# Optimization experiments

Measured on AMD Instinct MI355X. Metric: run time of the kernel, lower is better.

The kernel has to match this reference:

```python
import jax, jax.numpy as jnp
import numpy as np

B, M, L, D = 4, 128, 512, 768
NEG = -1e30


def setup_inputs() -> dict:
    key = jax.random.key(0)
    k1, k2 = jax.random.split(key)
    h = jax.random.normal(k1, (B, L, D), dtype=jnp.float32)
    mention_masks = jax.random.randint(k2, (B, M, L), 0, 2, dtype=jnp.int32)
    return {"h": h, "mention_masks": mention_masks}


def reference(h, mention_masks):
    # h: [B, L, D]; mention_masks: [B, M, L] (0/1)
    # Faithful to: m = (mask == 0).float() * -1e30; (m + h).max(dim=2)
    m = (mention_masks == 0).astype(h.dtype) * NEG          # [B, M, L]
    # broadcast add then max over token dim L -> [B, M, D]
    mention_reprs = jnp.max(h[:, None, :, :] + m[:, :, :, None], axis=2)
    return mention_reprs
```

## Files before the change

kernel.cpp:

```cpp
#include <hip/hip_runtime.h>

#define BB 4
#define MM 128
#define LL 512
#define DD 768
#define NEGF (-1e30f)

__global__ __launch_bounds__(256, 3) void mention_max_part(
    const float* __restrict__ h, const int* __restrict__ mask,
    float* __restrict__ ws)
{
    const int lane = threadIdx.x & 63;
    const int wave = threadIdx.x >> 6;
    const int dch  = blockIdx.x;
    const int mch  = blockIdx.y >> 2;
    const int lh   = blockIdx.y & 3;
    const int b    = blockIdx.z;

    const int d0 = dch * 256 + lane * 4;
    const int m0 = mch * 8;
    const int l0 = lh * 128 + wave * 32;

    const int lclamp = (l0 + lane < LL) ? (l0 + lane) : (LL - 1);
    const int* mp = mask + ((size_t)(b * MM + m0)) * LL + lclamp;

    unsigned bits[8];
#pragma unroll
    for (int m = 0; m < 8; ++m) {
        unsigned long long bl = __ballot(mp[m * LL] != 0);
        bits[m] = (unsigned)__builtin_amdgcn_readfirstlane((int)(unsigned)bl);
    }

    float4 acc[8];
#pragma unroll
    for (int m = 0; m < 8; ++m) acc[m] = make_float4(NEGF, NEGF, NEGF, NEGF);

#pragma unroll
    for (int s = 0; s < 2; ++s) {
        const float4* hp =
            (const float4*)(h + ((size_t)(b * LL + l0 + s * 16)) * DD + d0);
        float4 hreg[16];
#pragma unroll
        for (int i = 0; i < 16; ++i) hreg[i] = hp[(size_t)i * (DD / 4)];

#pragma unroll
        for (int m = 0; m < 8; ++m) {
            const unsigned w = bits[m];
            float4 a = acc[m];
#pragma unroll
            for (int i = 0; i < 16; i += 2) {
                const int k = s * 16 + i;
                const float ad0 = ((w >> k) & 1u) ? 0.0f : NEGF;
                const float ad1 = ((w >> (k + 1)) & 1u) ? 0.0f : NEGF;
                a.x = fmaxf(fmaxf(hreg[i].x + ad0, hreg[i + 1].x + ad1), a.x);
                a.y = fmaxf(fmaxf(hreg[i].y + ad0, hreg[i + 1].y + ad1), a.y);
                a.z = fmaxf(fmaxf(hreg[i].z + ad0, hreg[i + 1].z + ad1), a.z);
                a.w = fmaxf(fmaxf(hreg[i].w + ad0, hreg[i + 1].w + ad1), a.w);
            }
            acc[m] = a;
        }
    }

    __shared__ float4 red[4][8][64];
#pragma unroll
    for (int m = 0; m < 8; ++m) red[wave][m][lane] = acc[m];
    __syncthreads();

#pragma unroll
    for (int r = 0; r < 2; ++r) {
        const int o  = (int)threadIdx.x + r * 256;
        const int m  = o >> 6;
        const int dp = o & 63;
        float4 v = red[0][m][dp];
#pragma unroll
        for (int w = 1; w < 4; ++w) {
            const float4 u = red[w][m][dp];
            v.x = fmaxf(v.x, u.x);
            v.y = fmaxf(v.y, u.y);
            v.z = fmaxf(v.z, u.z);
            v.w = fmaxf(v.w, u.w);
        }
        ((float4*)(ws + ((size_t)lh * BB * MM * DD) +
                   ((size_t)(b * MM + m0 + m)) * DD + dch * 256))[dp] = v;
    }
}

__global__ __launch_bounds__(256) void mention_max_merge(
    const float* __restrict__ ws, float* __restrict__ out)
{
    const int i = (int)(blockIdx.x * blockDim.x + threadIdx.x);
    const size_t half = (size_t)BB * MM * DD;
    float4 v = ((const float4*)ws)[i];
#pragma unroll
    for (int p = 1; p < 4; ++p) {
        const float4 u = ((const float4*)(ws + p * half))[i];
        v.x = fmaxf(v.x, u.x);
        v.y = fmaxf(v.y, u.y);
        v.z = fmaxf(v.z, u.z);
        v.w = fmaxf(v.w, u.w);
    }
    ((float4*)out)[i] = v;
}

extern "C" void kernel_launch(void* const* d_in, const int* in_sizes, int n_in,
                              void* d_out, int out_size, void* d_ws, size_t ws_size,
                              hipStream_t stream) {
    const float* h    = (const float*)d_in[0];
    const int*   mask = (const int*)d_in[1];
    float*       out  = (float*)d_out;
    float*       ws   = (float*)d_ws;
    dim3 grid1(DD / 256, (MM / 8) * 4, BB);
    mention_max_part<<<grid1, dim3(256), 0, stream>>>(h, mask, ws);
    const int n4 = BB * MM * DD / 4;
    mention_max_merge<<<n4 / 256, dim3(256), 0, stream>>>(ws, out);
}
```

Before: 72.32 us.

## Split L into eight chunks, use LDS atomicMax reduction and scalar mask select

```diff
diff --git a/kernel.cpp b/kernel.cpp
--- a/kernel.cpp
+++ b/kernel.cpp
@@ -5,53 +5,79 @@
 #define LL 512
 #define DD 768
 #define NEGF (-1e30f)
+#define HALF  ((size_t)BB * MM * DD)
+#define HALF4 (HALF / 4)
 
-__global__ __launch_bounds__(256, 3) void mention_max_part(
+__device__ __forceinline__ unsigned enc(float x) {
+    int b = __float_as_int(x);
+    return (unsigned)(b ^ ((b >> 31) | 0x80000000));
+}
+__device__ __forceinline__ float dec(unsigned u) {
+    int b = (u & 0x80000000u) ? (int)(u ^ 0x80000000u) : ~(int)u;
+    return __int_as_float(b);
+}
+
+__global__ __launch_bounds__(256, 6) void mention_max_part(
     const float* __restrict__ h, const int* __restrict__ mask,
     float* __restrict__ ws)
 {
     const int lane = threadIdx.x & 63;
     const int wave = threadIdx.x >> 6;
     const int dch  = blockIdx.x;
-    const int mch  = blockIdx.y >> 2;
-    const int lh   = blockIdx.y & 3;
+    const int mch  = blockIdx.y >> 3;
+    const int lh   = blockIdx.y & 7;
     const int b    = blockIdx.z;
 
-    const int d0 = dch * 256 + lane * 4;
     const int m0 = mch * 8;
-    const int l0 = lh * 128 + wave * 32;
+    const int l0 = lh * 64 + wave * 16;
+    const int q  = lane >> 4;
+    const int lb = lane & 15;
 
-    const int lclamp = (l0 + lane < LL) ? (l0 + lane) : (LL - 1);
-    const int* mp = mask + ((size_t)(b * MM + m0)) * LL + lclamp;
+    __shared__ unsigned red[8][4][64];
+    for (int t = (int)threadIdx.x; t < 8 * 4 * 64; t += 256)
+        ((unsigned*)red)[t] = 0u;
 
-    unsigned bits[8];
+    const unsigned long long bal0 =
+        __ballot(mask[(size_t)(b * MM + m0 + q) * LL + l0 + lb] != 0);
+    const unsigned long long bal1 =
+        __ballot(mask[(size_t)(b * MM + m0 + 4 + q) * LL + l0 + lb] != 0);
+    unsigned w16[8];
 #pragma unroll
-    for (int m = 0; m < 8; ++m) {
-        unsigned long long bl = __ballot(mp[m * LL] != 0);
-        bits[m] = (unsigned)__builtin_amdgcn_readfirstlane((int)(unsigned)bl);
+    for (int m = 0; m < 4; ++m) {
+        w16[m]     = (unsigned)(bal0 >> (m * 16)) & 0xFFFFu;
+        w16[m + 4] = (unsigned)(bal1 >> (m * 16)) & 0xFFFFu;
     }
+
+    const unsigned negb = __float_as_uint(NEGF);
 
     float4 acc[8];
 #pragma unroll
     for (int m = 0; m < 8; ++m) acc[m] = make_float4(NEGF, NEGF, NEGF, NEGF);
 
+    const float4* hp = (const float4*)h +
+                       (size_t)(b * LL + l0) * (DD / 4) + dch * 64 + lane;
+
 #pragma unroll
     for (int s = 0; s < 2; ++s) {
-        const float4* hp =
-            (const float4*)(h + ((size_t)(b * LL + l0 + s * 16)) * DD + d0);
-        float4 hreg[16];
+        float4 hreg[8];
 #pragma unroll
-        for (int i = 0; i < 16; ++i) hreg[i] = hp[(size_t)i * (DD / 4)];
+        for (int i = 0; i < 8; ++i) hreg[i] = hp[(size_t)(s * 8 + i) * (DD / 4)];
 
 #pragma unroll
         for (int m = 0; m < 8; ++m) {
-            const unsigned w = bits[m];
+            const unsigned w = w16[m];
             float4 a = acc[m];
 #pragma unroll
-            for (int i = 0; i < 16; i += 2) {
-                const int k = s * 16 + i;
-                const float ad0 = ((w >> k) & 1u) ? 0.0f : NEGF;
-                const float ad1 = ((w >> (k + 1)) & 1u) ? 0.0f : NEGF;
+            for (int i = 0; i < 8; i += 2) {
+                unsigned adu0, adu1;
+                asm("s_bitcmp1_b32 %1, %2\n\t"
+                    "s_cselect_b32 %0, 0, %3"
+                    : "=s"(adu0) : "s"(w), "i"(s * 8 + i), "s"(negb) : "scc");
+                asm("s_bitcmp1_b32 %1, %2\n\t"
+                    "s_cselect_b32 %0, 0, %3"
+                    : "=s"(adu1) : "s"(w), "i"(s * 8 + i + 1), "s"(negb) : "scc");
+                const float ad0 = __uint_as_float(adu0);
+                const float ad1 = __uint_as_float(adu1);
                 a.x = fmaxf(fmaxf(hreg[i].x + ad0, hreg[i + 1].x + ad1), a.x);
                 a.y = fmaxf(fmaxf(hreg[i].y + ad0, hreg[i + 1].y + ad1), a.y);
                 a.z = fmaxf(fmaxf(hreg[i].z + ad0, hreg[i + 1].z + ad1), a.z);
@@ -61,9 +87,14 @@
         }
     }
 
-    __shared__ float4 red[4][8][64];
+    __syncthreads();
 #pragma unroll
-    for (int m = 0; m < 8; ++m) red[wave][m][lane] = acc[m];
+    for (int m = 0; m < 8; ++m) {
+        atomicMax(&red[m][0][lane], enc(acc[m].x));
+        atomicMax(&red[m][1][lane], enc(acc[m].y));
+        atomicMax(&red[m][2][lane], enc(acc[m].z));
+        atomicMax(&red[m][3][lane], enc(acc[m].w));
+    }
     __syncthreads();
 
 #pragma unroll
@@ -71,17 +102,13 @@
         const int o  = (int)threadIdx.x + r * 256;
         const int m  = o >> 6;
         const int dp = o & 63;
-        float4 v = red[0][m][dp];
-#pragma unroll
-        for (int w = 1; w < 4; ++w) {
-            const float4 u = red[w][m][dp];
-            v.x = fmaxf(v.x, u.x);
-            v.y = fmaxf(v.y, u.y);
-            v.z = fmaxf(v.z, u.z);
-            v.w = fmaxf(v.w, u.w);
-        }
-        ((float4*)(ws + ((size_t)lh * BB * MM * DD) +
-                   ((size_t)(b * MM + m0 + m)) * DD + dch * 256))[dp] = v;
+        float4 v;
+        v.x = dec(red[m][0][dp]);
+        v.y = dec(red[m][1][dp]);
+        v.z = dec(red[m][2][dp]);
+        v.w = dec(red[m][3][dp]);
+        ((float4*)ws)[(size_t)lh * HALF4 +
+                      (size_t)(b * MM + m0 + m) * (DD / 4) + dch * 64 + dp] = v;
     }
 }
 
@@ -89,11 +116,10 @@
     const float* __restrict__ ws, float* __restrict__ out)
 {
     const int i = (int)(blockIdx.x * blockDim.x + threadIdx.x);
-    const size_t half = (size_t)BB * MM * DD;
     float4 v = ((const float4*)ws)[i];
 #pragma unroll
-    for (int p = 1; p < 4; ++p) {
-        const float4 u = ((const float4*)(ws + p * half))[i];
+    for (int p = 1; p < 8; ++p) {
+        const float4 u = ((const float4*)ws)[(size_t)p * HALF4 + i];
         v.x = fmaxf(v.x, u.x);
         v.y = fmaxf(v.y, u.y);
         v.z = fmaxf(v.z, u.z);
@@ -109,7 +135,7 @@
     const int*   mask = (const int*)d_in[1];
     float*       out  = (float*)d_out;
     float*       ws   = (float*)d_ws;
-    dim3 grid1(DD / 256, (MM / 8) * 4, BB);
+    dim3 grid1(DD / 256, (MM / 8) * 8, BB);
     mention_max_part<<<grid1, dim3(256), 0, stream>>>(h, mask, ws);
     const int n4 = BB * MM * DD / 4;
     mention_max_merge<<<n4 / 256, dim3(256), 0, stream>>>(ws, out);
```

Result: no change. 73.09 us (+1.1%).
